# Optimization experiments

Measured on AMD Instinct MI355X. Metric: run time of the kernel, lower is better.

The kernel has to match this reference:

```python
import jax, jax.numpy as jnp
import numpy as np

N_USERS = 100_000
N_ITEMS = 50_000
N_NODES = N_USERS + N_ITEMS      # 150_000
EMB_DIM = 64
N_EDGES = 2_400_000              # avg degree ~16
N_LAYERS = 3
S_TEMP = 1.0                     # config['s_temp']


def segment_softmax(logits, seg, n):
    # numerically stable scatter-softmax over groups defined by seg
    m = jax.ops.segment_max(logits, seg, num_segments=n)
    e = jnp.exp(logits - m[seg])
    s = jax.ops.segment_sum(e, seg, num_segments=n)
    return e / s[seg]


def setup_inputs() -> dict:
    key = jax.random.key(0)
    k1, k2, k3 = jax.random.split(key, 3)
    emb_table = jax.random.normal(k1, (N_NODES, EMB_DIM), dtype=jnp.float32) * 0.1
    edge_index = jax.random.randint(k2, (2, N_EDGES), 0, N_NODES, dtype=jnp.int64)
    edge_attrs = jax.random.normal(k3, (N_EDGES,), dtype=jnp.float32)
    return {"emb_table": emb_table, "edge_index": edge_index, "edge_attrs": edge_attrs}


def reference(emb_table, edge_index, edge_attrs):
    frm, to = edge_index[0], edge_index[1]
    # DySimGCF edge normalization: geometric mean of incoming/outgoing scatter-softmax
    incoming = segment_softmax(edge_attrs / S_TEMP, to, N_NODES)
    outgoing = segment_softmax(edge_attrs / S_TEMP, frm, N_NODES)
    norm = jnp.sqrt(incoming * outgoing)          # [E]

    x = emb_table                                  # [N, D]
    embs = [x]
    for _ in range(N_LAYERS):
        # message = norm * x_j ; aggregate 'add' at destination == sparse mm
        msg = norm[:, None] * x[frm]               # [E, D]
        x = jax.ops.segment_sum(msg, to, num_segments=N_NODES)
        embs.append(x)
    # layer-average (lightGCN-style readout)
    out = jnp.mean(jnp.stack(embs, axis=1), axis=1)  # [N, D]
    return out
```

## Files before the change

### kernel.cpp

```cpp
#include <hip/hip_runtime.h>
#include <hip/hip_bf16.h>

#define N_NODES 150000
#define N_EDGES 2400000
#define DIM     64
#define MAXDEG  64

#define NB      256
#define NPB     587
#define NSHARD  4
#define CAPS    2816
#define BINBLK  512
#define BINTHR  512
#define EPB     ((N_EDGES + BINBLK - 1) / BINBLK)

__device__ __forceinline__ unsigned enc14(float v) {
    unsigned b = __float_as_uint(v);
    b += (1u << 13);
    int e5 = (int)((b >> 23) & 0xFF) - 104;
    if (e5 <= 0) return 0u;
    if (e5 > 31) e5 = 31;
    return ((unsigned)e5 << 9) | ((b >> 14) & 0x1FFu);
}
__device__ __forceinline__ float dec14(unsigned w) {
    return __uint_as_float((w << 14) + (104u << 23));
}
__device__ __forceinline__ unsigned packbf(float a, float b) {
    unsigned ua = __float_as_uint(a), ub = __float_as_uint(b);
    ua += 0x7FFFu + ((ua >> 16) & 1u);
    ub += 0x7FFFu + ((ub >> 16) & 1u);
    return (ua >> 16) | (ub & 0xFFFF0000u);
}
__device__ __forceinline__ float bflo(unsigned v) { return __uint_as_float(v << 16); }
__device__ __forceinline__ float bfhi(unsigned v) { return __uint_as_float(v & 0xFFFF0000u); }

__device__ __forceinline__ void scanNB(unsigned* scanBuf, int tid) {
    for (int off = 1; off < NB; off <<= 1) {
        unsigned v = 0u;
        if (tid < NB) { v = scanBuf[tid]; if (tid >= off) v += scanBuf[tid - off]; }
        __syncthreads();
        if (tid < NB) scanBuf[tid] = v;
        __syncthreads();
    }
}

__global__ __launch_bounds__(BINTHR) void binA_kernel(const float* __restrict__ attrs,
                                                      const int* __restrict__ frm,
                                                      const int* __restrict__ to,
                                                      unsigned* __restrict__ gcntT,
                                                      unsigned* __restrict__ gcntF,
                                                      uint2* __restrict__ recT,
                                                      unsigned* __restrict__ recF) {
    __shared__ unsigned hist[NB], baseL[NB], gBase[NB], cur[NB], scanBuf[NB];
    __shared__ uint2 bufT[EPB];
    unsigned* bufF = (unsigned*)bufT;

    int tid = threadIdx.x;
    int e0 = blockIdx.x * EPB;
    int e1 = e0 + EPB; if (e1 > N_EDGES) e1 = N_EDGES;
    int n = e1 - e0;
    unsigned shard = blockIdx.x & (NSHARD - 1);

    for (int i = tid; i < NB; i += BINTHR) { hist[i] = 0u; cur[i] = 0u; }
    __syncthreads();
    for (int e = e0 + tid; e < e1; e += BINTHR)
        atomicAdd(&hist[(unsigned)to[e] / NPB], 1u);
    __syncthreads();
    if (tid < NB) scanBuf[tid] = hist[tid];
    __syncthreads();
    scanNB(scanBuf, tid);
    if (tid < NB) {
        baseL[tid] = scanBuf[tid] - hist[tid];
        gBase[tid] = hist[tid] ? atomicAdd(&gcntT[tid * NSHARD + shard], hist[tid]) : 0u;
    }
    __syncthreads();
    for (int e = e0 + tid; e < e1; e += BINTHR) {
        unsigned t = (unsigned)to[e], f = (unsigned)frm[e];
        unsigned v14 = enc14(expf(attrs[e]));
        unsigned b = t / NPB;
        unsigned pos = baseL[b] + atomicAdd(&cur[b], 1u);
        bufT[pos] = make_uint2((t << 14) | v14, f);
    }
    __syncthreads();
    for (int s = tid; s < n; s += BINTHR) {
        uint2 r = bufT[s];
        unsigned b = (r.x >> 14) / NPB;
        unsigned dst = gBase[b] + ((unsigned)s - baseL[b]);
        if (dst < CAPS) recT[(size_t)(b * NSHARD + shard) * CAPS + dst] = r;
    }
    __syncthreads();

    for (int i = tid; i < NB; i += BINTHR) { hist[i] = 0u; cur[i] = 0u; }
    __syncthreads();
    for (int e = e0 + tid; e < e1; e += BINTHR)
        atomicAdd(&hist[(unsigned)frm[e] / NPB], 1u);
    __syncthreads();
    if (tid < NB) scanBuf[tid] = hist[tid];
    __syncthreads();
    scanNB(scanBuf, tid);
    if (tid < NB) {
        baseL[tid] = scanBuf[tid] - hist[tid];
        gBase[tid] = hist[tid] ? atomicAdd(&gcntF[tid * NSHARD + shard], hist[tid]) : 0u;
    }
    __syncthreads();
    for (int e = e0 + tid; e < e1; e += BINTHR) {
        unsigned f = (unsigned)frm[e];
        unsigned v14 = enc14(expf(attrs[e]));
        unsigned b = f / NPB;
        unsigned pos = baseL[b] + atomicAdd(&cur[b], 1u);
        bufF[pos] = (f << 14) | v14;
    }
    __syncthreads();
    for (int s = tid; s < n; s += BINTHR) {
        unsigned r = bufF[s];
        unsigned b = (r >> 14) / NPB;
        unsigned dst = gBase[b] + ((unsigned)s - baseL[b]);
        if (dst < CAPS) recF[(size_t)(b * NSHARD + shard) * CAPS + dst] = r;
    }
}

__global__ __launch_bounds__(1024) void sumF_kernel(const unsigned* __restrict__ recF,
                                                    const unsigned* __restrict__ gcntF,
                                                    float* __restrict__ s_out) {
    __shared__ float acc[NPB];
    int b = blockIdx.x;
    for (int i = threadIdx.x; i < NPB; i += blockDim.x) acc[i] = 0.f;
    __syncthreads();
    unsigned nodeBase = (unsigned)b * NPB;
    for (int s = 0; s < NSHARD; ++s) {
        unsigned n = gcntF[b * NSHARD + s];
        if (n > CAPS) n = CAPS;
        const unsigned* r = recF + (size_t)(b * NSHARD + s) * CAPS;
        for (unsigned i = threadIdx.x; i < n; i += blockDim.x) {
            unsigned w = r[i];
            atomicAdd(&acc[(w >> 14) - nodeBase], dec14(w & 0x3FFFu));
        }
    }
    __syncthreads();
    for (int i = threadIdx.x; i < NPB && (int)nodeBase + i < N_NODES; i += blockDim.x)
        s_out[nodeBase + i] = acc[i];
}

__global__ __launch_bounds__(1024) void buildT_kernel(const uint2* __restrict__ recT,
                                                      const unsigned* __restrict__ gcntT,
                                                      const float* __restrict__ s_out,
                                                      unsigned* __restrict__ edges,
                                                      int* __restrict__ fill) {
    __shared__ float    sinL[NPB];
    __shared__ unsigned filL[NPB];
    int b = blockIdx.x;
    for (int i = threadIdx.x; i < NPB; i += blockDim.x) { sinL[i] = 0.f; filL[i] = 0u; }
    __syncthreads();
    unsigned nodeBase = (unsigned)b * NPB;
    for (int s = 0; s < NSHARD; ++s) {
        unsigned n = gcntT[b * NSHARD + s];
        if (n > CAPS) n = CAPS;
        const uint2* r = recT + (size_t)(b * NSHARD + s) * CAPS;
        for (unsigned i = threadIdx.x; i < n; i += blockDim.x) {
            uint2 w = r[i];
            atomicAdd(&sinL[(w.x >> 14) - nodeBase], dec14(w.x & 0x3FFFu));
        }
    }
    __syncthreads();
    for (int s = 0; s < NSHARD; ++s) {
        unsigned n = gcntT[b * NSHARD + s];
        if (n > CAPS) n = CAPS;
        const uint2* r = recT + (size_t)(b * NSHARD + s) * CAPS;
        for (unsigned i = threadIdx.x; i < n; i += blockDim.x) {
            uint2 w = r[i];
            unsigned t = w.x >> 14;
            float ea = dec14(w.x & 0x3FFFu);
            unsigned f = w.y;
            float nrm = ea * rsqrtf(sinL[t - nodeBase] * s_out[f]);
            unsigned p = atomicAdd(&filL[t - nodeBase], 1u);
            if (p < MAXDEG) edges[(size_t)t * MAXDEG + p] = (f << 14) | enc14(nrm);
        }
    }
    __syncthreads();
    for (int i = threadIdx.x; i < NPB && (int)nodeBase + i < N_NODES; i += blockDim.x) {
        unsigned n = filL[i]; if (n > MAXDEG) n = MAXDEG;
        unsigned n8 = (n + 7u) & ~7u; if (n8 > MAXDEG) n8 = MAXDEG;
        for (unsigned p = n; p < n8; ++p)
            edges[(size_t)(nodeBase + i) * MAXDEG + p] = 0u;
        fill[nodeBase + i] = (int)n8;
    }
}

__global__ __launch_bounds__(256) void cvt_kernel(const float* __restrict__ emb,
                                                  unsigned* __restrict__ embB) {
    int i = blockIdx.x * blockDim.x + threadIdx.x;
    if (i >= N_NODES * DIM / 4) return;
    float4 v = reinterpret_cast<const float4*>(emb)[i];
    uint2 p;
    p.x = packbf(v.x, v.y);
    p.y = packbf(v.z, v.w);
    reinterpret_cast<uint2*>(embB)[i] = p;
}

#define QSEL(W, V4) { unsigned t1_ = (q & 1) ? (V4).y : (V4).x; \
                      unsigned t2_ = (q & 1) ? (V4).w : (V4).z; \
                      W = (q & 2) ? t2_ : t1_; }
#define QFMA(N, X) { ax += (N) * bflo((X).x); ay += (N) * bfhi((X).x); \
                     az += (N) * bflo((X).y); aw_ += (N) * bfhi((X).y); }

template<bool FINAL>
__global__ __launch_bounds__(256) void layer_kernel(const uint2* __restrict__ xw2,
                                                    const unsigned* __restrict__ edges,
                                                    const int* __restrict__ fill,
                                                    uint2* __restrict__ yw2,
                                                    const uint2* __restrict__ embB2,
                                                    const uint2* __restrict__ x1w2,
                                                    const uint2* __restrict__ x2w2,
                                                    float* __restrict__ out) {
    int node = blockIdx.x * 4 + (threadIdx.x >> 6);
    int nodeU = __builtin_amdgcn_readfirstlane(node);
    int lane = threadIdx.x & 63;
    int q  = lane >> 4;
    int p4 = lane & 15;
    int cnt = fill[nodeU];
    const uint4* erow4 = reinterpret_cast<const uint4*>(edges + (size_t)nodeU * MAXDEG);
    float ax = 0.f, ay = 0.f, az = 0.f, aw_ = 0.f;
    if (cnt > 0) {
        uint4 A = erow4[0], B = erow4[1];
        unsigned w0, w1;
        QSEL(w0, A); QSEL(w1, B);
        uint2 xa = xw2[(w0 >> 14) * 16 + p4];
        uint2 xb = xw2[(w1 >> 14) * 16 + p4];
        float n0 = dec14(w0 & 0x3FFFu), n1 = dec14(w1 & 0x3FFFu);
        for (int j = 8; j < cnt; j += 8) {
            uint4 A1 = erow4[j >> 2], B1 = erow4[(j >> 2) + 1];
            unsigned v0, v1;
            QSEL(v0, A1); QSEL(v1, B1);
            uint2 xc = xw2[(v0 >> 14) * 16 + p4];
            uint2 xd = xw2[(v1 >> 14) * 16 + p4];
            float m0 = dec14(v0 & 0x3FFFu), m1 = dec14(v1 & 0x3FFFu);
            QFMA(n0, xa); QFMA(n1, xb);
            n0 = m0; n1 = m1; xa = xc; xb = xd;
        }
        QFMA(n0, xa); QFMA(n1, xb);
    }
    ax += __shfl_xor(ax, 16, 64); ay += __shfl_xor(ay, 16, 64);
    az += __shfl_xor(az, 16, 64); aw_ += __shfl_xor(aw_, 16, 64);
    ax += __shfl_xor(ax, 32, 64); ay += __shfl_xor(ay, 32, 64);
    az += __shfl_xor(az, 32, 64); aw_ += __shfl_xor(aw_, 32, 64);
    if (lane < 16) {
        int o = nodeU * 16 + p4;
        if (!FINAL) {
            yw2[o] = make_uint2(packbf(ax, ay), packbf(az, aw_));
        } else {
            uint2 e = embB2[o], u1 = x1w2[o], u2 = x2w2[o];
            float4 r;
            r.x = 0.25f * (bflo(e.x) + bflo(u1.x) + bflo(u2.x) + ax);
            r.y = 0.25f * (bfhi(e.x) + bfhi(u1.x) + bfhi(u2.x) + ay);
            r.z = 0.25f * (bflo(e.y) + bflo(u1.y) + bflo(u2.y) + az);
            r.w = 0.25f * (bfhi(e.y) + bfhi(u1.y) + bfhi(u2.y) + aw_);
            reinterpret_cast<float4*>(out)[o] = r;
        }
    }
}

extern "C" void kernel_launch(void* const* d_in, const int* in_sizes, int n_in,
                              void* d_out, int out_size, void* d_ws, size_t ws_size,
                              hipStream_t stream) {
    const float* emb   = (const float*)d_in[0];
    const int*   eidx  = (const int*)d_in[1];
    const float* attrs = (const float*)d_in[2];
    const int* frm = eidx;
    const int* to  = eidx + N_EDGES;
    float* out = (float*)d_out;

    float*    s_out = (float*)d_ws;
    int*      fill  = (int*)(s_out + N_NODES);
    unsigned* gcntT = (unsigned*)(fill + N_NODES);
    unsigned* gcntF = gcntT + NB * NSHARD;
    unsigned* edges = gcntF + NB * NSHARD;
    unsigned* embB  = edges + (size_t)N_NODES * MAXDEG;
    unsigned* U     = embB + (size_t)N_NODES * 32;
    uint2*    recT  = (uint2*)U;
    unsigned* recF  = (unsigned*)(recT + (size_t)NB * NSHARD * CAPS);
    unsigned* xA    = U;
    unsigned* xB    = xA + (size_t)N_NODES * 32;

    const int B = 256;
    const int gV4 = (N_NODES * DIM / 4 + B - 1) / B;
    const int gN  = N_NODES / 4;

    hipMemsetAsync(gcntT, 0, 2 * NB * NSHARD * sizeof(unsigned), stream);
    binA_kernel<<<BINBLK, BINTHR, 0, stream>>>(attrs, frm, to, gcntT, gcntF, recT, recF);
    sumF_kernel<<<NB, 1024, 0, stream>>>(recF, gcntF, s_out);
    buildT_kernel<<<NB, 1024, 0, stream>>>(recT, gcntT, s_out, edges, fill);
    cvt_kernel<<<gV4, B, 0, stream>>>(emb, embB);

    const uint2* embB2 = (const uint2*)embB;
    uint2* xA2 = (uint2*)xA;
    uint2* xB2 = (uint2*)xB;

    layer_kernel<false><<<gN, B, 0, stream>>>(embB2, edges, fill, xA2,
                                              embB2, xA2, xB2, out);
    layer_kernel<false><<<gN, B, 0, stream>>>((const uint2*)xA, edges, fill, xB2,
                                              embB2, xA2, xB2, out);
    layer_kernel<true ><<<gN, B, 0, stream>>>((const uint2*)xB, edges, fill, xA2,
                                              embB2, xA2, xB2, out);
}
```

Measured before the change: 262.3 us.

## Fuse to/from binning passes and widen layer gather to 16-byte loads

```diff
diff --git a/kernel.cpp b/kernel.cpp
--- a/kernel.cpp
+++ b/kernel.cpp
@@ -34,16 +34,6 @@
 __device__ __forceinline__ float bflo(unsigned v) { return __uint_as_float(v << 16); }
 __device__ __forceinline__ float bfhi(unsigned v) { return __uint_as_float(v & 0xFFFF0000u); }
 
-__device__ __forceinline__ void scanNB(unsigned* scanBuf, int tid) {
-    for (int off = 1; off < NB; off <<= 1) {
-        unsigned v = 0u;
-        if (tid < NB) { v = scanBuf[tid]; if (tid >= off) v += scanBuf[tid - off]; }
-        __syncthreads();
-        if (tid < NB) scanBuf[tid] = v;
-        __syncthreads();
-    }
-}
-
 __global__ __launch_bounds__(BINTHR) void binA_kernel(const float* __restrict__ attrs,
                                                       const int* __restrict__ frm,
                                                       const int* __restrict__ to,
@@ -51,9 +41,10 @@
                                                       unsigned* __restrict__ gcntF,
                                                       uint2* __restrict__ recT,
                                                       unsigned* __restrict__ recF) {
-    __shared__ unsigned hist[NB], baseL[NB], gBase[NB], cur[NB], scanBuf[NB];
-    __shared__ uint2 bufT[EPB];
-    unsigned* bufF = (unsigned*)bufT;
+    __shared__ unsigned histT[NB], histF[NB], baseT[NB], baseF[NB];
+    __shared__ unsigned gBaseT[NB], gBaseF[NB], curT[NB], curF[NB];
+    __shared__ uint2    bufT[EPB];
+    __shared__ unsigned bufF[EPB];
 
     int tid = threadIdx.x;
     int e0 = blockIdx.x * EPB;
@@ -61,60 +52,58 @@
     int n = e1 - e0;
     unsigned shard = blockIdx.x & (NSHARD - 1);
 
-    for (int i = tid; i < NB; i += BINTHR) { hist[i] = 0u; cur[i] = 0u; }
-    __syncthreads();
-    for (int e = e0 + tid; e < e1; e += BINTHR)
-        atomicAdd(&hist[(unsigned)to[e] / NPB], 1u);
-    __syncthreads();
-    if (tid < NB) scanBuf[tid] = hist[tid];
-    __syncthreads();
-    scanNB(scanBuf, tid);
+    for (int i = tid; i < NB; i += BINTHR) {
+        histT[i] = 0u; histF[i] = 0u; curT[i] = 0u; curF[i] = 0u;
+    }
+    __syncthreads();
+
+    for (int e = e0 + tid; e < e1; e += BINTHR) {
+        atomicAdd(&histT[(unsigned)to[e] / NPB], 1u);
+        atomicAdd(&histF[(unsigned)frm[e] / NPB], 1u);
+    }
+    __syncthreads();
+
+    if (tid < NB) { baseT[tid] = histT[tid]; baseF[tid] = histF[tid]; }
+    __syncthreads();
+    for (int off = 1; off < NB; off <<= 1) {
+        unsigned vT = 0u, vF = 0u;
+        if (tid < NB) {
+            vT = baseT[tid]; vF = baseF[tid];
+            if (tid >= off) { vT += baseT[tid - off]; vF += baseF[tid - off]; }
+        }
+        __syncthreads();
+        if (tid < NB) { baseT[tid] = vT; baseF[tid] = vF; }
+        __syncthreads();
+    }
     if (tid < NB) {
-        baseL[tid] = scanBuf[tid] - hist[tid];
-        gBase[tid] = hist[tid] ? atomicAdd(&gcntT[tid * NSHARD + shard], hist[tid]) : 0u;
-    }
-    __syncthreads();
+        unsigned hT = histT[tid], hF = histF[tid];
+        baseT[tid] -= hT;
+        baseF[tid] -= hF;
+        gBaseT[tid] = hT ? atomicAdd(&gcntT[tid * NSHARD + shard], hT) : 0u;
+        gBaseF[tid] = hF ? atomicAdd(&gcntF[tid * NSHARD + shard], hF) : 0u;
+    }
+    __syncthreads();
+
     for (int e = e0 + tid; e < e1; e += BINTHR) {
         unsigned t = (unsigned)to[e], f = (unsigned)frm[e];
         unsigned v14 = enc14(expf(attrs[e]));
-        unsigned b = t / NPB;
-        unsigned pos = baseL[b] + atomicAdd(&cur[b], 1u);
-        bufT[pos] = make_uint2((t << 14) | v14, f);
-    }
-    __syncthreads();
+        unsigned bT = t / NPB;
+        bufT[baseT[bT] + atomicAdd(&curT[bT], 1u)] = make_uint2((t << 14) | v14, f);
+        unsigned bF = f / NPB;
+        bufF[baseF[bF] + atomicAdd(&curF[bF], 1u)] = (f << 14) | v14;
+    }
+    __syncthreads();
+
     for (int s = tid; s < n; s += BINTHR) {
         uint2 r = bufT[s];
         unsigned b = (r.x >> 14) / NPB;
-        unsigned dst = gBase[b] + ((unsigned)s - baseL[b]);
+        unsigned dst = gBaseT[b] + ((unsigned)s - baseT[b]);
         if (dst < CAPS) recT[(size_t)(b * NSHARD + shard) * CAPS + dst] = r;
     }
-    __syncthreads();
-
-    for (int i = tid; i < NB; i += BINTHR) { hist[i] = 0u; cur[i] = 0u; }
-    __syncthreads();
-    for (int e = e0 + tid; e < e1; e += BINTHR)
-        atomicAdd(&hist[(unsigned)frm[e] / NPB], 1u);
-    __syncthreads();
-    if (tid < NB) scanBuf[tid] = hist[tid];
-    __syncthreads();
-    scanNB(scanBuf, tid);
-    if (tid < NB) {
-        baseL[tid] = scanBuf[tid] - hist[tid];
-        gBase[tid] = hist[tid] ? atomicAdd(&gcntF[tid * NSHARD + shard], hist[tid]) : 0u;
-    }
-    __syncthreads();
-    for (int e = e0 + tid; e < e1; e += BINTHR) {
-        unsigned f = (unsigned)frm[e];
-        unsigned v14 = enc14(expf(attrs[e]));
-        unsigned b = f / NPB;
-        unsigned pos = baseL[b] + atomicAdd(&cur[b], 1u);
-        bufF[pos] = (f << 14) | v14;
-    }
-    __syncthreads();
     for (int s = tid; s < n; s += BINTHR) {
         unsigned r = bufF[s];
         unsigned b = (r >> 14) / NPB;
-        unsigned dst = gBase[b] + ((unsigned)s - baseL[b]);
+        unsigned dst = gBaseF[b] + ((unsigned)s - baseF[b]);
         if (dst < CAPS) recF[(size_t)(b * NSHARD + shard) * CAPS + dst] = r;
     }
 }
@@ -197,64 +186,92 @@
     reinterpret_cast<uint2*>(embB)[i] = p;
 }
 
-#define QSEL(W, V4) { unsigned t1_ = (q & 1) ? (V4).y : (V4).x; \
-                      unsigned t2_ = (q & 1) ? (V4).w : (V4).z; \
-                      W = (q & 2) ? t2_ : t1_; }
-#define QFMA(N, X) { ax += (N) * bflo((X).x); ay += (N) * bfhi((X).x); \
-                     az += (N) * bflo((X).y); aw_ += (N) * bfhi((X).y); }
+#define QSEL8(W, A, B) { unsigned t1_ = (q & 1) ? (A).y : (A).x; \
+                         unsigned t2_ = (q & 1) ? (A).w : (A).z; \
+                         unsigned wa_ = (q & 2) ? t2_ : t1_; \
+                         unsigned t3_ = (q & 1) ? (B).y : (B).x; \
+                         unsigned t4_ = (q & 1) ? (B).w : (B).z; \
+                         unsigned wb_ = (q & 2) ? t4_ : t3_; \
+                         W = (q & 4) ? wb_ : wa_; }
+#define UFMA(N, X) { a0 += (N) * bflo((X).x); a1 += (N) * bfhi((X).x); \
+                     a2 += (N) * bflo((X).y); a3 += (N) * bfhi((X).y); \
+                     a4 += (N) * bflo((X).z); a5 += (N) * bfhi((X).z); \
+                     a6 += (N) * bflo((X).w); a7 += (N) * bfhi((X).w); }
 
 template<bool FINAL>
-__global__ __launch_bounds__(256) void layer_kernel(const uint2* __restrict__ xw2,
+__global__ __launch_bounds__(256) void layer_kernel(const uint4* __restrict__ xw4,
                                                     const unsigned* __restrict__ edges,
                                                     const int* __restrict__ fill,
-                                                    uint2* __restrict__ yw2,
-                                                    const uint2* __restrict__ embB2,
-                                                    const uint2* __restrict__ x1w2,
-                                                    const uint2* __restrict__ x2w2,
+                                                    uint4* __restrict__ yw4,
+                                                    const uint4* __restrict__ embB4,
+                                                    const uint4* __restrict__ x1w4,
+                                                    const uint4* __restrict__ x2w4,
                                                     float* __restrict__ out) {
     int node = blockIdx.x * 4 + (threadIdx.x >> 6);
     int nodeU = __builtin_amdgcn_readfirstlane(node);
     int lane = threadIdx.x & 63;
-    int q  = lane >> 4;
-    int p4 = lane & 15;
+    int q  = lane >> 3;
+    int p8 = lane & 7;
     int cnt = fill[nodeU];
     const uint4* erow4 = reinterpret_cast<const uint4*>(edges + (size_t)nodeU * MAXDEG);
-    float ax = 0.f, ay = 0.f, az = 0.f, aw_ = 0.f;
-    if (cnt > 0) {
-        uint4 A = erow4[0], B = erow4[1];
-        unsigned w0, w1;
-        QSEL(w0, A); QSEL(w1, B);
-        uint2 xa = xw2[(w0 >> 14) * 16 + p4];
-        uint2 xb = xw2[(w1 >> 14) * 16 + p4];
-        float n0 = dec14(w0 & 0x3FFFu), n1 = dec14(w1 & 0x3FFFu);
-        for (int j = 8; j < cnt; j += 8) {
-            uint4 A1 = erow4[j >> 2], B1 = erow4[(j >> 2) + 1];
-            unsigned v0, v1;
-            QSEL(v0, A1); QSEL(v1, B1);
-            uint2 xc = xw2[(v0 >> 14) * 16 + p4];
-            uint2 xd = xw2[(v1 >> 14) * 16 + p4];
-            float m0 = dec14(v0 & 0x3FFFu), m1 = dec14(v1 & 0x3FFFu);
-            QFMA(n0, xa); QFMA(n1, xb);
-            n0 = m0; n1 = m1; xa = xc; xb = xd;
-        }
-        QFMA(n0, xa); QFMA(n1, xb);
-    }
-    ax += __shfl_xor(ax, 16, 64); ay += __shfl_xor(ay, 16, 64);
-    az += __shfl_xor(az, 16, 64); aw_ += __shfl_xor(aw_, 16, 64);
-    ax += __shfl_xor(ax, 32, 64); ay += __shfl_xor(ay, 32, 64);
-    az += __shfl_xor(az, 32, 64); aw_ += __shfl_xor(aw_, 32, 64);
-    if (lane < 16) {
-        int o = nodeU * 16 + p4;
+    float a0 = 0.f, a1 = 0.f, a2 = 0.f, a3 = 0.f;
+    float a4 = 0.f, a5 = 0.f, a6 = 0.f, a7 = 0.f;
+    int nIter = cnt >> 3;
+    if (nIter > 0) {
+        uint4 A0 = erow4[0], B0 = erow4[1];
+        unsigned w0;
+        QSEL8(w0, A0, B0);
+        uint4 xa = xw4[(w0 >> 14) * 8 + p8];
+        unsigned w1 = 0u;
+        uint4 xb = make_uint4(0u, 0u, 0u, 0u);
+        if (nIter > 1) {
+            uint4 A1 = erow4[2], B1 = erow4[3];
+            QSEL8(w1, A1, B1);
+            xb = xw4[(w1 >> 14) * 8 + p8];
+        }
+        for (int g = 2; g < nIter; ++g) {
+            uint4 A2 = erow4[2 * g], B2 = erow4[2 * g + 1];
+            unsigned w2;
+            QSEL8(w2, A2, B2);
+            uint4 xc = xw4[(w2 >> 14) * 8 + p8];
+            float n0 = dec14(w0 & 0x3FFFu);
+            UFMA(n0, xa);
+            w0 = w1; xa = xb;
+            w1 = w2; xb = xc;
+        }
+        { float n0 = dec14(w0 & 0x3FFFu); UFMA(n0, xa); }
+        if (nIter > 1) { float n1 = dec14(w1 & 0x3FFFu); UFMA(n1, xb); }
+    }
+    a0 += __shfl_xor(a0, 8, 64);  a1 += __shfl_xor(a1, 8, 64);
+    a2 += __shfl_xor(a2, 8, 64);  a3 += __shfl_xor(a3, 8, 64);
+    a4 += __shfl_xor(a4, 8, 64);  a5 += __shfl_xor(a5, 8, 64);
+    a6 += __shfl_xor(a6, 8, 64);  a7 += __shfl_xor(a7, 8, 64);
+    a0 += __shfl_xor(a0, 16, 64); a1 += __shfl_xor(a1, 16, 64);
+    a2 += __shfl_xor(a2, 16, 64); a3 += __shfl_xor(a3, 16, 64);
+    a4 += __shfl_xor(a4, 16, 64); a5 += __shfl_xor(a5, 16, 64);
+    a6 += __shfl_xor(a6, 16, 64); a7 += __shfl_xor(a7, 16, 64);
+    a0 += __shfl_xor(a0, 32, 64); a1 += __shfl_xor(a1, 32, 64);
+    a2 += __shfl_xor(a2, 32, 64); a3 += __shfl_xor(a3, 32, 64);
+    a4 += __shfl_xor(a4, 32, 64); a5 += __shfl_xor(a5, 32, 64);
+    a6 += __shfl_xor(a6, 32, 64); a7 += __shfl_xor(a7, 32, 64);
+    if (lane < 8) {
+        int o = nodeU * 8 + p8;
         if (!FINAL) {
-            yw2[o] = make_uint2(packbf(ax, ay), packbf(az, aw_));
+            yw4[o] = make_uint4(packbf(a0, a1), packbf(a2, a3),
+                                packbf(a4, a5), packbf(a6, a7));
         } else {
-            uint2 e = embB2[o], u1 = x1w2[o], u2 = x2w2[o];
-            float4 r;
-            r.x = 0.25f * (bflo(e.x) + bflo(u1.x) + bflo(u2.x) + ax);
-            r.y = 0.25f * (bfhi(e.x) + bfhi(u1.x) + bfhi(u2.x) + ay);
-            r.z = 0.25f * (bflo(e.y) + bflo(u1.y) + bflo(u2.y) + az);
-            r.w = 0.25f * (bfhi(e.y) + bfhi(u1.y) + bfhi(u2.y) + aw_);
-            reinterpret_cast<float4*>(out)[o] = r;
+            uint4 e = embB4[o], u1 = x1w4[o], u2 = x2w4[o];
+            float4 r0, r1;
+            r0.x = 0.25f * (bflo(e.x) + bflo(u1.x) + bflo(u2.x) + a0);
+            r0.y = 0.25f * (bfhi(e.x) + bfhi(u1.x) + bfhi(u2.x) + a1);
+            r0.z = 0.25f * (bflo(e.y) + bflo(u1.y) + bflo(u2.y) + a2);
+            r0.w = 0.25f * (bfhi(e.y) + bfhi(u1.y) + bfhi(u2.y) + a3);
+            r1.x = 0.25f * (bflo(e.z) + bflo(u1.z) + bflo(u2.z) + a4);
+            r1.y = 0.25f * (bfhi(e.z) + bfhi(u1.z) + bfhi(u2.z) + a5);
+            r1.z = 0.25f * (bflo(e.w) + bflo(u1.w) + bflo(u2.w) + a6);
+            r1.w = 0.25f * (bfhi(e.w) + bfhi(u1.w) + bfhi(u2.w) + a7);
+            reinterpret_cast<float4*>(out)[2 * o]     = r0;
+            reinterpret_cast<float4*>(out)[2 * o + 1] = r1;
         }
     }
 }
@@ -291,14 +308,14 @@
     buildT_kernel<<<NB, 1024, 0, stream>>>(recT, gcntT, s_out, edges, fill);
     cvt_kernel<<<gV4, B, 0, stream>>>(emb, embB);
 
-    const uint2* embB2 = (const uint2*)embB;
-    uint2* xA2 = (uint2*)xA;
-    uint2* xB2 = (uint2*)xB;
-
-    layer_kernel<false><<<gN, B, 0, stream>>>(embB2, edges, fill, xA2,
-                                              embB2, xA2, xB2, out);
-    layer_kernel<false><<<gN, B, 0, stream>>>((const uint2*)xA, edges, fill, xB2,
-                                              embB2, xA2, xB2, out);
-    layer_kernel<true ><<<gN, B, 0, stream>>>((const uint2*)xB, edges, fill, xA2,
-                                              embB2, xA2, xB2, out);
-}
+    const uint4* embB4 = (const uint4*)embB;
+    uint4* xA4 = (uint4*)xA;
+    uint4* xB4 = (uint4*)xB;
+
+    layer_kernel<false><<<gN, B, 0, stream>>>(embB4, edges, fill, xA4,
+                                              embB4, xA4, xB4, out);
+    layer_kernel<false><<<gN, B, 0, stream>>>((const uint4*)xA, edges, fill, xB4,
+                                              embB4, xA4, xB4, out);
+    layer_kernel<true ><<<gN, B, 0, stream>>>((const uint4*)xB, edges, fill, xA4,
+                                              embB4, xA4, xB4, out);
+}
```

Result: faster. 253.2 us (-3.4%).
